# Kernel optimization log

Hardware: AMD Instinct MI355X
Metric: run time of the kernel (lower is better)

Reference implementation:

```python
import jax, jax.numpy as jnp
import numpy as np

EPS = 1e-6
ALPHA = 0.2  # LeakyReLU negative slope


def layer_norm(x, g, b):
    mu = jnp.mean(x, axis=-1, keepdims=True)
    var = jnp.mean(jnp.square(x - mu), axis=-1, keepdims=True)
    return (x - mu) * jax.lax.rsqrt(var + EPS) * g + b


def graph_attention(x, bias, W, a_src, a_dst):
    # x: [B,N,D], bias: [B,N,N], W: [D, H*Dh], a_src/a_dst: [H, Dh]
    B, N, D = x.shape
    H, Dh = a_src.shape
    h = jnp.einsum('bnd,dhk->bhnk', x, W.reshape(D, H, Dh))  # [B,H,N,Dh]
    s = jnp.einsum('bhnk,hk->bhn', h, a_src)                 # source term
    t = jnp.einsum('bhnk,hk->bhn', h, a_dst)                 # target term
    e = jax.nn.leaky_relu(s[:, :, :, None] + t[:, :, None, :], ALPHA)
    e = e + bias[:, None, :, :]                              # graph mask/bias
    attn = jax.nn.softmax(e, axis=-1)                        # [B,H,N,N]
    out = jnp.einsum('bhij,bhjk->bhik', attn, h)             # [B,H,N,Dh]
    return out.transpose(0, 2, 1, 3).reshape(B, N, H * Dh)


def setup_inputs() -> dict:
    key = jax.random.key(0)
    ks = jax.random.split(key, 8)
    B, N, D, H = 2, 2048, 512, 8
    Dh = D // H
    sc = 1.0 / np.sqrt(D)
    return {
        'x': jax.random.normal(ks[0], (B, N, D), jnp.float32),
        'bias': jax.random.normal(ks[1], (B, N, N), jnp.float32),
        'W1': jax.random.normal(ks[2], (D, D), jnp.float32) * sc,
        'a_src1': jax.random.normal(ks[3], (H, Dh), jnp.float32) * sc,
        'a_dst1': jax.random.normal(ks[4], (H, Dh), jnp.float32) * sc,
        'g1': jnp.ones((D,), jnp.float32),
        'b1': jnp.zeros((D,), jnp.float32),
        'W2': jax.random.normal(ks[5], (D, D), jnp.float32) * sc,
        'a_src2': jax.random.normal(ks[6], (1, D), jnp.float32) * sc,
        'a_dst2': jax.random.normal(ks[7], (1, D), jnp.float32) * sc,
        'g2': jnp.ones((D,), jnp.float32),
        'b2': jnp.zeros((D,), jnp.float32),
    }


def reference(x, bias, W1, a_src1, a_dst1, g1, b1, W2, a_src2, a_dst2, g2, b2):
    # dropout is identity in eval mode
    attn_in = layer_norm(x, g1, b1)
    attn = graph_attention(attn_in, bias, W1, a_src1, a_dst1) + x
    attn_in2 = layer_norm(attn, g2, b2)
    out = graph_attention(attn_in2, bias, W2, a_src2, a_dst2) + attn
    return out
```

## Files before the change

kernel.cpp:

```cpp
#include <hip/hip_runtime.h>
#include <math.h>

#define NB 2
#define NN 2048
#define DD 512
#define L2E 1.44269504088896340736f

typedef __attribute__((ext_vector_type(8))) short short8;
typedef __attribute__((ext_vector_type(4))) float f32x4;

__device__ __forceinline__ unsigned short f2bf(float x) {
  union { float f; unsigned u; } a;
  a.f = x;
  unsigned r = a.u + 0x7FFF + ((a.u >> 16) & 1);
  return (unsigned short)(r >> 16);
}
__device__ __forceinline__ float bf2f(unsigned short u) {
  union { unsigned u; float f; } a;
  a.u = ((unsigned)u) << 16;
  return a.f;
}
__device__ __forceinline__ unsigned cvtpk(float lo, float hi) {
  unsigned r;
  asm("v_cvt_pk_bf16_f32 %0, %1, %2" : "=v"(r) : "v"(lo), "v"(hi));
  return r;
}
__device__ __forceinline__ uint2 exp4pk(float e0, float e1, float e2, float e3) {
  float p0, p1, p2, p3;
  uint2 d;
  asm("v_exp_f32 %2, %6\n\t"
      "v_exp_f32 %3, %7\n\t"
      "v_exp_f32 %4, %8\n\t"
      "v_exp_f32 %5, %9\n\t"
      "v_cvt_pk_bf16_f32 %0, %2, %3\n\t"
      "v_cvt_pk_bf16_f32 %1, %4, %5"
      : "=&v"(d.x), "=&v"(d.y), "=&v"(p0), "=&v"(p1), "=&v"(p2), "=&v"(p3)
      : "v"(e0), "v"(e1), "v"(e2), "v"(e3));
  return d;
}

__device__ __forceinline__ float waveReduceSum(float v) {
#pragma unroll
  for (int o = 32; o; o >>= 1) v += __shfl_down(v, o, 64);
  return v;
}
__device__ __forceinline__ float blockReduceSum(float v, float* red4) {
  int tid = threadIdx.x;
  __syncthreads();
  v = waveReduceSum(v);
  if ((tid & 63) == 0) red4[tid >> 6] = v;
  __syncthreads();
  return red4[0] + red4[1] + red4[2] + red4[3];
}

__global__ __launch_bounds__(256) void prep_kernel(
    const float* __restrict__ W1, const float* __restrict__ W2,
    unsigned short* __restrict__ WT1, unsigned short* __restrict__ WT2,
    const float* __restrict__ as1, const float* __restrict__ ad1,
    float* __restrict__ vs1, float* __restrict__ vd1,
    const float* __restrict__ as2, const float* __restrict__ ad2,
    float* __restrict__ vs2, float* __restrict__ vd2) {
  __shared__ float tile[64][65];
  int bid = blockIdx.x;
  int t = threadIdx.x;
  if (bid < 128) {
    const float* W = (bid & 64) ? W2 : W1;
    unsigned short* WT = (bid & 64) ? WT2 : WT1;
    int r = bid & 63;
    int kt = (r >> 3) * 64, ct = (r & 7) * 64;
#pragma unroll
    for (int u = 0; u < 16; u++) {
      int lin = t + u * 256;
      int kl = lin >> 6, cl = lin & 63;
      tile[kl][cl] = W[(size_t)(kt + kl) * DD + ct + cl];
    }
    __syncthreads();
#pragma unroll
    for (int u = 0; u < 16; u++) {
      int lin = t + u * 256;
      int cl = lin >> 6, kl = lin & 63;
      WT[(size_t)(ct + cl) * DD + kt + kl] = f2bf(tile[kl][cl]);
    }
  } else {
    int idx = bid - 128;
    int slot = idx >> 3, dch = idx & 7;
    const float *W, *as, *ad;
    float *vs, *vd;
    int Dh, hoff;
    if (slot < 8) {
      W = W1; as = as1 + slot * 64; ad = ad1 + slot * 64;
      vs = vs1 + (size_t)slot * DD; vd = vd1 + (size_t)slot * DD;
      Dh = 64; hoff = slot * 64;
    } else {
      W = W2; as = as2; ad = ad2; vs = vs2; vd = vd2;
      Dh = 512; hoff = 0;
    }
    int dl = t >> 2, kq = t & 3;
    int d = dch * 64 + dl;
    int kn = Dh >> 2;
    const float* wr = W + (size_t)d * DD + hoff + kq * kn;
    const float* asp = as + kq * kn;
    const float* adp = ad + kq * kn;
    float s = 0.f, dd2 = 0.f;
    for (int k = 0; k < kn; k++) {
      float wv = wr[k];
      s += wv * asp[k];
      dd2 += wv * adp[k];
    }
    s += __shfl_xor(s, 1);
    s += __shfl_xor(s, 2);
    dd2 += __shfl_xor(dd2, 1);
    dd2 += __shfl_xor(dd2, 2);
    if (kq == 0) {
      vs[d] = s;
      vd[d] = dd2;
    }
  }
}

__global__ __launch_bounds__(256) void lnst_kernel(
    const float* __restrict__ x, const float* __restrict__ g,
    const float* __restrict__ bb, unsigned short* __restrict__ y,
    const float* __restrict__ vs, const float* __restrict__ vd,
    float* __restrict__ sOut, float* __restrict__ tOut, int HN) {
  __shared__ float red4[4];
  __shared__ float lnS[512];
  int row = blockIdx.x;
  int t = threadIdx.x;
  const float* xr = x + (size_t)row * DD;
  float2 v = *(const float2*)&xr[2 * t];
  float s = blockReduceSum(v.x + v.y, red4);
  float mu = s * (1.0f / 512.0f);
  float d0 = v.x - mu, d1 = v.y - mu;
  float ss = blockReduceSum(d0 * d0 + d1 * d1, red4);
  float rstd = rsqrtf(ss * (1.0f / 512.0f) + 1e-6f);
  float2 gg = *(const float2*)&g[2 * t];
  float2 bv = *(const float2*)&bb[2 * t];
  float n0 = d0 * rstd * gg.x + bv.x;
  float n1 = d1 * rstd * gg.y + bv.y;
  ushort2 o;
  o.x = f2bf(n0);
  o.y = f2bf(n1);
  *(ushort2*)&y[(size_t)row * DD + 2 * t] = o;
  lnS[2 * t] = n0;
  lnS[2 * t + 1] = n1;
  __syncthreads();
  int wv = t >> 6, l = t & 63;
  int b = row >> 11, n = row & (NN - 1);
  float4 x0 = *(const float4*)&lnS[l * 8];
  float4 x1 = *(const float4*)&lnS[l * 8 + 4];
  for (int h = wv; h < HN; h += 4) {
    const float* vsr = vs + (size_t)h * DD + l * 8;
    const float* vdr = vd + (size_t)h * DD + l * 8;
    float4 a0 = *(const float4*)vsr, a1 = *(const float4*)(vsr + 4);
    float4 c0 = *(const float4*)vdr, c1 = *(const float4*)(vdr + 4);
    float ps = x0.x * a0.x + x0.y * a0.y + x0.z * a0.z + x0.w * a0.w +
               x1.x * a1.x + x1.y * a1.y + x1.z * a1.z + x1.w * a1.w;
    float pd = x0.x * c0.x + x0.y * c0.y + x0.z * c0.z + x0.w * c0.w +
               x1.x * c1.x + x1.y * c1.y + x1.z * c1.z + x1.w * c1.w;
#pragma unroll
    for (int o2 = 32; o2; o2 >>= 1) {
      ps += __shfl_xor(ps, o2);
      pd += __shfl_xor(pd, o2);
    }
    if (l == 0) {
      sOut[((size_t)b * HN + h) * NN + n] = ps * L2E;
      tOut[((size_t)b * HN + h) * NN + n] = pd * L2E;
    }
  }
}

__global__ __launch_bounds__(256) void gemm_kernel(const unsigned short* __restrict__ A,
                                                   const unsigned short* __restrict__ BT,
                                                   unsigned short* __restrict__ hbT) {
  __shared__ float accL[4][16][65];
  int t = threadIdx.x, w = t >> 6, l = t & 63;
  int li = l & 15, lg = l >> 4;
  int R0 = blockIdx.x * 16;
  int c0 = blockIdx.y * 64;
  const unsigned short* ar = A + (size_t)(R0 + li) * DD + w * 128 + lg * 8;
  const unsigned short* br = BT + (size_t)(c0 + li) * DD + w * 128 + lg * 8;
  f32x4 acc[4] = {};
#pragma unroll
  for (int k0 = 0; k0 < 128; k0 += 32) {
    short8 af = *(const short8*)(ar + k0);
#pragma unroll
    for (int f = 0; f < 4; f++) {
      short8 bf = *(const short8*)(br + (size_t)f * 16 * DD + k0);
      acc[f] = __builtin_amdgcn_mfma_f32_16x16x32_bf16(af, bf, acc[f], 0, 0, 0);
    }
  }
#pragma unroll
  for (int f = 0; f < 4; f++)
#pragma unroll
    for (int r = 0; r < 4; r++) accL[w][lg * 4 + r][f * 16 + li] = acc[f][r];
  __syncthreads();
  int b = R0 >> 11, jT = (R0 & (NN - 1)) >> 4;
#pragma unroll
  for (int u = 0; u < 2; u++) {
    int idx = t + u * 256;
    int f = idx >> 7;
    int rem = idx & 127;
    int cl = rem >> 3, jlp = rem & 7;
    int cc = f * 16 + cl;
    float v0 = accL[0][2 * jlp][cc] + accL[1][2 * jlp][cc] + accL[2][2 * jlp][cc] +
               accL[3][2 * jlp][cc];
    float v1 = accL[0][2 * jlp + 1][cc] + accL[1][2 * jlp + 1][cc] +
               accL[2][2 * jlp + 1][cc] + accL[3][2 * jlp + 1][cc];
    size_t off = (((size_t)(b * (DD / 64) + blockIdx.y) * (NN / 16)) + jT) * 1024 +
                 f * 256 + cl * 16 + jlp * 2;
    *(unsigned*)(hbT + off) = cvtpk(v0, v1);
  }
}

__global__ __launch_bounds__(1024) void pvh_kernel(
    const unsigned short* __restrict__ hbT, const float* __restrict__ bias,
    const float* __restrict__ sArr, const float* __restrict__ tArr,
    const float* __restrict__ res, float* __restrict__ out) {
  __shared__ __align__(16) unsigned char smem[65536];
  unsigned short (*Pl)[2][1024] = (unsigned short (*)[2][1024])smem;
  int t = threadIdx.x, w = t >> 6, l = t & 63;
  int h = w & 7, jh = w >> 3;
  int li = l & 15, lg = l >> 4;
  int i0g = blockIdx.x * 16;
  int b = i0g >> 11, i0 = i0g & (NN - 1);
  size_t bhN = (size_t)(b * 8 + h) * NN;
  const float* trow = tArr + bhN;

  int rs = l >> 3, js = (l & 7) * 8, jc = l & 7;
  int wchunk = ((jc & 4) | ((jc & 3) ^ (rs & 3))) * 8;
  float sv[2];
  sv[0] = sArr[bhN + i0 + rs];
  sv[1] = sArr[bhN + i0 + 8 + rs];
  const float* bb0 = bias + ((size_t)b * NN + i0 + rs) * NN;
  const float* bb1 = bb0 + (size_t)8 * NN;

  const unsigned short* vbase =
      hbT + ((size_t)(b * 8 + h) * (NN / 16)) * 1024 + (lg >> 1) * 1024 + li * 16 +
      (lg & 1) * 8;
  int ra0 = li * 64 + (lg ^ (li & 3)) * 8;
  int ra1 = ra0 + 32;

  union { short8 v; unsigned short q[8]; } ones;
#pragma unroll
  for (int k = 0; k < 8; k++) ones.q[k] = 0x3F80;

  f32x4 acc[4] = {};
  f32x4 accS = {0.f, 0.f, 0.f, 0.f};

  auto loadTB = [&](int j, float4& t0, float4& t1, float4& b0a, float4& b0b,
                    float4& b1a, float4& b1b) {
    t0 = *(const float4*)&trow[j + js];
    t1 = *(const float4*)&trow[j + js + 4];
    b0a = *(const float4*)&bb0[j + js];
    b0b = *(const float4*)&bb0[j + js + 4];
    b1a = *(const float4*)&bb1[j + js];
    b1b = *(const float4*)&bb1[j + js + 4];
  };
  auto computeP = [&](const float4& t0, const float4& t1, const float4& b0a,
                      const float4& b0b, const float4& b1a, const float4& b1b, int pb) {
#pragma unroll
    for (int u = 0; u < 2; u++) {
      const float4& ba = u ? b1a : b0a;
      const float4& bc = u ? b1b : b0b;
      int row = u * 8 + rs;
      float e0 = sv[u] + t0.x, e1 = sv[u] + t0.y;
      float e2 = sv[u] + t0.z, e3 = sv[u] + t0.w;
      float e4 = sv[u] + t1.x, e5 = sv[u] + t1.y;
      float e6 = sv[u] + t1.z, e7 = sv[u] + t1.w;
      e0 = fmaf(ba.x, L2E, fmaxf(e0, 0.2f * e0));
      e1 = fmaf(ba.y, L2E, fmaxf(e1, 0.2f * e1));
      e2 = fmaf(ba.z, L2E, fmaxf(e2, 0.2f * e2));
      e3 = fmaf(ba.w, L2E, fmaxf(e3, 0.2f * e3));
      e4 = fmaf(bc.x, L2E, fmaxf(e4, 0.2f * e4));
      e5 = fmaf(bc.y, L2E, fmaxf(e5, 0.2f * e5));
      e6 = fmaf(bc.z, L2E, fmaxf(e6, 0.2f * e6));
      e7 = fmaf(bc.w, L2E, fmaxf(e7, 0.2f * e7));
      uint2 d0 = exp4pk(e0, e1, e2, e3);
      uint2 d1 = exp4pk(e4, e5, e6, e7);
      uint4 dd;
      dd.x = d0.x; dd.y = d0.y; dd.z = d1.x; dd.w = d1.y;
      *(uint4*)&Pl[w][pb][rs * 64 + u * 512 + wchunk] = dd;
    }
  };

  const int jbeg = jh * (NN / 2), jend = jbeg + NN / 2;
  float4 tA0, tA1, bA0, bA1, bA2, bA3;

  loadTB(jbeg, tA0, tA1, bA0, bA1, bA2, bA3);
  computeP(tA0, tA1, bA0, bA1, bA2, bA3, 0);
  loadTB(jbeg + 64, tA0, tA1, bA0, bA1, bA2, bA3);

  int buf = 0;
  for (int jt = jbeg; jt < jend; jt += 64) {
    const unsigned short* vp = vbase + (size_t)jt * 64;
    short8 v0 = *(const short8*)(vp + 0);
    short8 v1 = *(const short8*)(vp + 256);
    short8 v2 = *(const short8*)(vp + 512);
    short8 v3 = *(const short8*)(vp + 768);
    short8 v4 = *(const short8*)(vp + 2048);
    short8 v5 = *(const short8*)(vp + 2304);
    short8 v6 = *(const short8*)(vp + 2560);
    short8 v7 = *(const short8*)(vp + 2816);
    short8 a0 = *(const short8*)&Pl[w][buf][(li & 7) * 64 + (li >> 3) * 512 +
                                            ((lg ^ (li & 3)) * 8)];
    short8 a1 = *(const short8*)&Pl[w][buf][(li & 7) * 64 + (li >> 3) * 512 + 32 +
                                            ((lg ^ (li & 3)) * 8)];
    if (jt + 64 < jend) {
      float4 n0 = tA0, n1 = tA1, m0 = bA0, m1 = bA1, m2 = bA2, m3 = bA3;
      int jn = (jt + 128 < jend) ? (jt + 128) : jbeg;
      loadTB(jn, tA0, tA1, bA0, bA1, bA2, bA3);
      computeP(n0, n1, m0, m1, m2, m3, buf ^ 1);
    }
    __builtin_amdgcn_s_setprio(1);
    accS = __builtin_amdgcn_mfma_f32_16x16x32_bf16(a0, ones.v, accS, 0, 0, 0);
    acc[0] = __builtin_amdgcn_mfma_f32_16x16x32_bf16(a0, v0, acc[0], 0, 0, 0);
    acc[1] = __builtin_amdgcn_mfma_f32_16x16x32_bf16(a0, v1, acc[1], 0, 0, 0);
    acc[2] = __builtin_amdgcn_mfma_f32_16x16x32_bf16(a0, v2, acc[2], 0, 0, 0);
    acc[3] = __builtin_amdgcn_mfma_f32_16x16x32_bf16(a0, v3, acc[3], 0, 0, 0);
    accS = __builtin_amdgcn_mfma_f32_16x16x32_bf16(a1, ones.v, accS, 0, 0, 0);
    acc[0] = __builtin_amdgcn_mfma_f32_16x16x32_bf16(a1, v4, acc[0], 0, 0, 0);
    acc[1] = __builtin_amdgcn_mfma_f32_16x16x32_bf16(a1, v5, acc[1], 0, 0, 0);
    acc[2] = __builtin_amdgcn_mfma_f32_16x16x32_bf16(a1, v6, acc[2], 0, 0, 0);
    acc[3] = __builtin_amdgcn_mfma_f32_16x16x32_bf16(a1, v7, acc[3], 0, 0, 0);
    __builtin_amdgcn_s_setprio(0);
    buf ^= 1;
  }

  __syncthreads();
  float* mAcc = (float*)smem;
  float* mS = (float*)(smem + 8 * 16 * 68 * 4);
  if (jh == 1) {
#pragma unroll
    for (int f = 0; f < 4; f++)
#pragma unroll
      for (int r = 0; r < 4; r++)
        mAcc[((size_t)h * 16 + lg * 4 + r) * 68 + f * 16 + li] = acc[f][r];
    if (li == 0) {
#pragma unroll
      for (int r = 0; r < 4; r++) mS[h * 16 + lg * 4 + r] = accS[r];
    }
  }
  __syncthreads();
  if (jh == 0) {
#pragma unroll
    for (int r = 0; r < 4; r++) {
      float S = accS[r] + mS[h * 16 + lg * 4 + r];
      float inv = 1.0f / S;
      size_t ix = ((size_t)b * NN + i0 + lg * 4 + r) * DD + h * 64 + li;
#pragma unroll
      for (int f = 0; f < 4; f++) {
        float O = acc[f][r] + mAcc[((size_t)h * 16 + lg * 4 + r) * 68 + f * 16 + li];
        out[ix + f * 16] = O * inv + res[ix + f * 16];
      }
    }
  }
}

template <int HN, int CCH>
__global__ __launch_bounds__(256) void pv_kernel(
    const unsigned short* __restrict__ hbT, const float* __restrict__ bias,
    const float* __restrict__ sArr, const float* __restrict__ tArr,
    const float* __restrict__ res, float* __restrict__ out) {
  constexpr int DH = DD / HN;
  __shared__ unsigned short Pl[4][2][1024];
  __shared__ float accL[4][16][33];
  __shared__ float sLa[4][16];
  int t = threadIdx.x, w = t >> 6, l = t & 63;
  int li = l & 15, lg = l >> 4;
  int i0 = blockIdx.x * 16;
  int ck = blockIdx.y, bh = blockIdx.z;
  int h = bh % HN, b = bh / HN;
  int c0 = h * DH + ck * (CCH * 64);
  size_t bhN = (size_t)bh * NN;
  const float* trow = tArr + bhN;

  int rs = l >> 3, js = (l & 7) * 8, jc = l & 7;
  int wchunk = ((jc & 4) | ((jc & 3) ^ (rs & 3))) * 8;
  float sv[2];
  sv[0] = sArr[bhN + i0 + rs];
  sv[1] = sArr[bhN + i0 + 8 + rs];
  const float* bb0 = bias + ((size_t)b * NN + i0 + rs) * NN;
  const float* bb1 = bb0 + (size_t)8 * NN;

  const unsigned short* vbase =
      hbT + ((size_t)(b * (DD / 64) + (c0 >> 6)) * (NN / 16)) * 1024 +
      (lg >> 1) * 1024 + li * 16 + (lg & 1) * 8;
  int ra0 = li * 64 + (lg ^ (li & 3)) * 8;
  int ra1 = ra0 + 32;

  union { short8 v; unsigned short q[8]; } ones;
#pragma unroll
  for (int k = 0; k < 8; k++) ones.q[k] = 0x3F80;

  const int jbeg = w * (NN / 4), jend = jbeg + NN / 4;
  f32x4 acc[CCH][4] = {};
  f32x4 accS = {0.f, 0.f, 0.f, 0.f};

  auto loadTB = [&](int j, float4& t0, float4& t1, float4& b0a, float4& b0b,
                    float4& b1a, float4& b1b) {
    t0 = *(const float4*)&trow[j + js];
    t1 = *(const float4*)&trow[j + js + 4];
    b0a = *(const float4*)&bb0[j + js];
    b0b = *(const float4*)&bb0[j + js + 4];
    b1a = *(const float4*)&bb1[j + js];
    b1b = *(const float4*)&bb1[j + js + 4];
  };
  auto computeP = [&](const float4& t0, const float4& t1, const float4& b0a,
                      const float4& b0b, const float4& b1a, const float4& b1b, int pb) {
#pragma unroll
    for (int u = 0; u < 2; u++) {
      const float4& ba = u ? b1a : b0a;
      const float4& bc = u ? b1b : b0b;
      int row = u * 8 + rs;
      float e0 = sv[u] + t0.x, e1 = sv[u] + t0.y;
      float e2 = sv[u] + t0.z, e3 = sv[u] + t0.w;
      float e4 = sv[u] + t1.x, e5 = sv[u] + t1.y;
      float e6 = sv[u] + t1.z, e7 = sv[u] + t1.w;
      e0 = fmaf(ba.x, L2E, fmaxf(e0, 0.2f * e0));
      e1 = fmaf(ba.y, L2E, fmaxf(e1, 0.2f * e1));
      e2 = fmaf(ba.z, L2E, fmaxf(e2, 0.2f * e2));
      e3 = fmaf(ba.w, L2E, fmaxf(e3, 0.2f * e3));
      e4 = fmaf(bc.x, L2E, fmaxf(e4, 0.2f * e4));
      e5 = fmaf(bc.y, L2E, fmaxf(e5, 0.2f * e5));
      e6 = fmaf(bc.z, L2E, fmaxf(e6, 0.2f * e6));
      e7 = fmaf(bc.w, L2E, fmaxf(e7, 0.2f * e7));
      uint2 d0 = exp4pk(e0, e1, e2, e3);
      uint2 d1 = exp4pk(e4, e5, e6, e7);
      uint4 dd;
      dd.x = d0.x; dd.y = d0.y; dd.z = d1.x; dd.w = d1.y;
      *(uint4*)&Pl[w][pb][row * 64 + wchunk] = dd;
    }
  };

  float4 tA0, tA1, bA0, bA1, bA2, bA3;

  loadTB(jbeg, tA0, tA1, bA0, bA1, bA2, bA3);
  computeP(tA0, tA1, bA0, bA1, bA2, bA3, 0);
  loadTB(jbeg + 64, tA0, tA1, bA0, bA1, bA2, bA3);

  int buf = 0;
  for (int jt = jbeg; jt < jend; jt += 64) {
    short8 a0 = *(const short8*)&Pl[w][buf][ra0];
    short8 a1 = *(const short8*)&Pl[w][buf][ra1];
    if (jt + 64 < jend) {
      float4 n0 = tA0, n1 = tA1, m0 = bA0, m1 = bA1, m2 = bA2, m3 = bA3;
      int jn = (jt + 128 < jend) ? (jt + 128) : jbeg;
      loadTB(jn, tA0, tA1, bA0, bA1, bA2, bA3);
      computeP(n0, n1, m0, m1, m2, m3, buf ^ 1);
    }
    __builtin_amdgcn_s_setprio(1);
    accS = __builtin_amdgcn_mfma_f32_16x16x32_bf16(a0, ones.v, accS, 0, 0, 0);
    accS = __builtin_amdgcn_mfma_f32_16x16x32_bf16(a1, ones.v, accS, 0, 0, 0);
#pragma unroll
    for (int cc = 0; cc < CCH; cc++) {
      const unsigned short* vp =
          vbase + (size_t)cc * ((NN / 16) * 1024) + (size_t)jt * 64;
      short8 v0 = *(const short8*)(vp + 0);
      short8 v1 = *(const short8*)(vp + 256);
      short8 v2 = *(const short8*)(vp + 512);
      short8 v3 = *(const short8*)(vp + 768);
      acc[cc][0] = __builtin_amdgcn_mfma_f32_16x16x32_bf16(a0, v0, acc[cc][0], 0, 0, 0);
      acc[cc][1] = __builtin_amdgcn_mfma_f32_16x16x32_bf16(a0, v1, acc[cc][1], 0, 0, 0);
      acc[cc][2] = __builtin_amdgcn_mfma_f32_16x16x32_bf16(a0, v2, acc[cc][2], 0, 0, 0);
      acc[cc][3] = __builtin_amdgcn_mfma_f32_16x16x32_bf16(a0, v3, acc[cc][3], 0, 0, 0);
      short8 v4 = *(const short8*)(vp + 2048);
      short8 v5 = *(const short8*)(vp + 2304);
      short8 v6 = *(const short8*)(vp + 2560);
      short8 v7 = *(const short8*)(vp + 2816);
      acc[cc][0] = __builtin_amdgcn_mfma_f32_16x16x32_bf16(a1, v4, acc[cc][0], 0, 0, 0);
      acc[cc][1] = __builtin_amdgcn_mfma_f32_16x16x32_bf16(a1, v5, acc[cc][1], 0, 0, 0);
      acc[cc][2] = __builtin_amdgcn_mfma_f32_16x16x32_bf16(a1, v6, acc[cc][2], 0, 0, 0);
      acc[cc][3] = __builtin_amdgcn_mfma_f32_16x16x32_bf16(a1, v7, acc[cc][3], 0, 0, 0);
    }
    __builtin_amdgcn_s_setprio(0);
    buf ^= 1;
  }

  if (li == 0) {
#pragma unroll
    for (int r = 0; r < 4; r++) sLa[w][lg * 4 + r] = accS[r];
  }
#pragma unroll
  for (int g = 0; g < 2 * CCH; g++) {
    int cc = g >> 1, half = g & 1;
#pragma unroll
    for (int f = 0; f < 2; f++)
#pragma unroll
      for (int r = 0; r < 4; r++)
        accL[w][lg * 4 + r][f * 16 + li] = acc[cc][half * 2 + f][r];
    __syncthreads();
    {
      int rr = t >> 4, cp = (t & 15) * 2;
      float S = sLa[0][rr] + sLa[1][rr] + sLa[2][rr] + sLa[3][rr];
      float inv = 1.0f / S;
      float2 O = {0.f, 0.f};
#pragma unroll
      for (int w2 = 0; w2 < 4; w2++) {
        O.x += accL[w2][rr][cp];
        O.y += accL[w2][rr][cp + 1];
      }
      size_t ix = ((size_t)b * NN + i0 + rr) * DD + c0 + cc * 64 + half * 32 + cp;
      float2 rv = *(const float2*)&res[ix];
      float2 ov = {O.x * inv + rv.x, O.y * inv + rv.y};
      *(float2*)&out[ix] = ov;
    }
    __syncthreads();
  }
}

extern "C" void kernel_launch(void* const* d_in, const int* in_sizes, int n_in,
                              void* d_out, int out_size, void* d_ws, size_t ws_size,
                              hipStream_t stream) {
  const float* x = (const float*)d_in[0];
  const float* bias = (const float*)d_in[1];
  const float* W1 = (const float*)d_in[2];
  const float* asrc1 = (const float*)d_in[3];
  const float* adst1 = (const float*)d_in[4];
  const float* g1 = (const float*)d_in[5];
  const float* b1 = (const float*)d_in[6];
  const float* W2 = (const float*)d_in[7];
  const float* asrc2 = (const float*)d_in[8];
  const float* adst2 = (const float*)d_in[9];
  const float* g2 = (const float*)d_in[10];
  const float* b2 = (const float*)d_in[11];
  float* out = (float*)d_out;
  float* ws = (float*)d_ws;

  const size_t RC = (size_t)NB * NN * DD;
  float* attnBuf = ws;
  unsigned short* lnB = (unsigned short*)(ws + RC);
  unsigned short* hbT = (unsigned short*)(ws + RC + RC / 2);
  unsigned short* WT1 = (unsigned short*)(ws + 2 * RC);
  unsigned short* WT2 = WT1 + (size_t)DD * DD;
  float* vs1 = (float*)(WT2 + (size_t)DD * DD);
  float* vd1 = vs1 + 8 * DD;
  float* vs2 = vd1 + 8 * DD;
  float* vd2 = vs2 + DD;
  float* sBuf = vd2 + DD;
  float* tBuf = sBuf + 16 * NN;

  const int rows = NB * NN;

  hipLaunchKernelGGL(prep_kernel, dim3(128 + 72), dim3(256), 0, stream, W1, W2, WT1, WT2,
                     asrc1, adst1, vs1, vd1, asrc2, adst2, vs2, vd2);

  hipLaunchKernelGGL(lnst_kernel, dim3(rows), dim3(256), 0, stream, x, g1, b1, lnB, vs1, vd1,
                     sBuf, tBuf, 8);
  hipLaunchKernelGGL(gemm_kernel, dim3(256, 8), dim3(256), 0, stream, lnB, WT1, hbT);
  hipLaunchKernelGGL(pvh_kernel, dim3(256), dim3(1024), 0, stream, hbT, bias, sBuf, tBuf, x,
                     attnBuf);

  hipLaunchKernelGGL(lnst_kernel, dim3(rows), dim3(256), 0, stream, attnBuf, g2, b2, lnB, vs2,
                     vd2, sBuf, tBuf, 1);
  hipLaunchKernelGGL(gemm_kernel, dim3(256, 8), dim3(256), 0, stream, lnB, WT2, hbT);
  hipLaunchKernelGGL((pv_kernel<1, 4>), dim3(128, 2, 2), dim3(256), 0, stream, hbT, bias,
                     sBuf, tBuf, attnBuf, out);
}
```

Measured before the change: 174.0 us.

## Split attention kernels into smaller 256-thread blocks across heads and channel chunks

The first-layer attention kernel goes from 1024-thread blocks covering all 8 heads to 256-thread blocks covering 2 heads each, on a 3D grid with less shared memory. The second-layer kernel halves the channel chunk per block (CCH 4 to 2) and doubles the grid. It also prefetches all V fragments before the MFMAs and reuses the P buffer space for the reduction. This is meant to raise occupancy and block count so the SMs fill better and memory latency is hidden. The cost is recomputing the softmax weights (bias reads and exps) across more blocks, which means more bias traffic.

Result: faster. 152.2 us, median of 3 (-12.6%).

```diff
diff --git a/kernel.cpp b/kernel.cpp
--- a/kernel.cpp
+++ b/kernel.cpp
@@ -213,18 +213,21 @@
   }
 }
 
-__global__ __launch_bounds__(1024) void pvh_kernel(
+__global__ __launch_bounds__(256) void pvg_kernel(
     const unsigned short* __restrict__ hbT, const float* __restrict__ bias,
     const float* __restrict__ sArr, const float* __restrict__ tArr,
     const float* __restrict__ res, float* __restrict__ out) {
-  __shared__ __align__(16) unsigned char smem[65536];
+  __shared__ __align__(16) unsigned char smem[16896];
   unsigned short (*Pl)[2][1024] = (unsigned short (*)[2][1024])smem;
+  float (*accL2)[16][65] = (float (*)[16][65])smem;
+  float (*sLa)[16] = (float (*)[16])(smem + 8320);
   int t = threadIdx.x, w = t >> 6, l = t & 63;
-  int h = w & 7, jh = w >> 3;
+  int jh = w & 1, hp = w >> 1;
   int li = l & 15, lg = l >> 4;
-  int i0g = blockIdx.x * 16;
-  int b = i0g >> 11, i0 = i0g & (NN - 1);
-  size_t bhN = (size_t)(b * 8 + h) * NN;
+  int i0 = blockIdx.x * 16;
+  int h0 = blockIdx.y * 2, b = blockIdx.z;
+  int head = h0 + hp;
+  size_t bhN = (size_t)(b * 8 + head) * NN;
   const float* trow = tArr + bhN;
 
   int rs = l >> 3, js = (l & 7) * 8, jc = l & 7;
@@ -236,7 +239,7 @@
   const float* bb1 = bb0 + (size_t)8 * NN;
 
   const unsigned short* vbase =
-      hbT + ((size_t)(b * 8 + h) * (NN / 16)) * 1024 + (lg >> 1) * 1024 + li * 16 +
+      hbT + ((size_t)(b * 8 + head) * (NN / 16)) * 1024 + (lg >> 1) * 1024 + li * 16 +
       (lg & 1) * 8;
   int ra0 = li * 64 + (lg ^ (li & 3)) * 8;
   int ra1 = ra0 + 32;
@@ -245,156 +248,8 @@
 #pragma unroll
   for (int k = 0; k < 8; k++) ones.q[k] = 0x3F80;
 
+  const int jbeg = jh * (NN / 2), jend = jbeg + NN / 2;
   f32x4 acc[4] = {};
-  f32x4 accS = {0.f, 0.f, 0.f, 0.f};
-
-  auto loadTB = [&](int j, float4& t0, float4& t1, float4& b0a, float4& b0b,
-                    float4& b1a, float4& b1b) {
-    t0 = *(const float4*)&trow[j + js];
-    t1 = *(const float4*)&trow[j + js + 4];
-    b0a = *(const float4*)&bb0[j + js];
-    b0b = *(const float4*)&bb0[j + js + 4];
-    b1a = *(const float4*)&bb1[j + js];
-    b1b = *(const float4*)&bb1[j + js + 4];
-  };
-  auto computeP = [&](const float4& t0, const float4& t1, const float4& b0a,
-                      const float4& b0b, const float4& b1a, const float4& b1b, int pb) {
-#pragma unroll
-    for (int u = 0; u < 2; u++) {
-      const float4& ba = u ? b1a : b0a;
-      const float4& bc = u ? b1b : b0b;
-      int row = u * 8 + rs;
-      float e0 = sv[u] + t0.x, e1 = sv[u] + t0.y;
-      float e2 = sv[u] + t0.z, e3 = sv[u] + t0.w;
-      float e4 = sv[u] + t1.x, e5 = sv[u] + t1.y;
-      float e6 = sv[u] + t1.z, e7 = sv[u] + t1.w;
-      e0 = fmaf(ba.x, L2E, fmaxf(e0, 0.2f * e0));
-      e1 = fmaf(ba.y, L2E, fmaxf(e1, 0.2f * e1));
-      e2 = fmaf(ba.z, L2E, fmaxf(e2, 0.2f * e2));
-      e3 = fmaf(ba.w, L2E, fmaxf(e3, 0.2f * e3));
-      e4 = fmaf(bc.x, L2E, fmaxf(e4, 0.2f * e4));
-      e5 = fmaf(bc.y, L2E, fmaxf(e5, 0.2f * e5));
-      e6 = fmaf(bc.z, L2E, fmaxf(e6, 0.2f * e6));
-      e7 = fmaf(bc.w, L2E, fmaxf(e7, 0.2f * e7));
-      uint2 d0 = exp4pk(e0, e1, e2, e3);
-      uint2 d1 = exp4pk(e4, e5, e6, e7);
-      uint4 dd;
-      dd.x = d0.x; dd.y = d0.y; dd.z = d1.x; dd.w = d1.y;
-      *(uint4*)&Pl[w][pb][rs * 64 + u * 512 + wchunk] = dd;
-    }
-  };
-
-  const int jbeg = jh * (NN / 2), jend = jbeg + NN / 2;
-  float4 tA0, tA1, bA0, bA1, bA2, bA3;
-
-  loadTB(jbeg, tA0, tA1, bA0, bA1, bA2, bA3);
-  computeP(tA0, tA1, bA0, bA1, bA2, bA3, 0);
-  loadTB(jbeg + 64, tA0, tA1, bA0, bA1, bA2, bA3);
-
-  int buf = 0;
-  for (int jt = jbeg; jt < jend; jt += 64) {
-    const unsigned short* vp = vbase + (size_t)jt * 64;
-    short8 v0 = *(const short8*)(vp + 0);
-    short8 v1 = *(const short8*)(vp + 256);
-    short8 v2 = *(const short8*)(vp + 512);
-    short8 v3 = *(const short8*)(vp + 768);
-    short8 v4 = *(const short8*)(vp + 2048);
-    short8 v5 = *(const short8*)(vp + 2304);
-    short8 v6 = *(const short8*)(vp + 2560);
-    short8 v7 = *(const short8*)(vp + 2816);
-    short8 a0 = *(const short8*)&Pl[w][buf][(li & 7) * 64 + (li >> 3) * 512 +
-                                            ((lg ^ (li & 3)) * 8)];
-    short8 a1 = *(const short8*)&Pl[w][buf][(li & 7) * 64 + (li >> 3) * 512 + 32 +
-                                            ((lg ^ (li & 3)) * 8)];
-    if (jt + 64 < jend) {
-      float4 n0 = tA0, n1 = tA1, m0 = bA0, m1 = bA1, m2 = bA2, m3 = bA3;
-      int jn = (jt + 128 < jend) ? (jt + 128) : jbeg;
-      loadTB(jn, tA0, tA1, bA0, bA1, bA2, bA3);
-      computeP(n0, n1, m0, m1, m2, m3, buf ^ 1);
-    }
-    __builtin_amdgcn_s_setprio(1);
-    accS = __builtin_amdgcn_mfma_f32_16x16x32_bf16(a0, ones.v, accS, 0, 0, 0);
-    acc[0] = __builtin_amdgcn_mfma_f32_16x16x32_bf16(a0, v0, acc[0], 0, 0, 0);
-    acc[1] = __builtin_amdgcn_mfma_f32_16x16x32_bf16(a0, v1, acc[1], 0, 0, 0);
-    acc[2] = __builtin_amdgcn_mfma_f32_16x16x32_bf16(a0, v2, acc[2], 0, 0, 0);
-    acc[3] = __builtin_amdgcn_mfma_f32_16x16x32_bf16(a0, v3, acc[3], 0, 0, 0);
-    accS = __builtin_amdgcn_mfma_f32_16x16x32_bf16(a1, ones.v, accS, 0, 0, 0);
-    acc[0] = __builtin_amdgcn_mfma_f32_16x16x32_bf16(a1, v4, acc[0], 0, 0, 0);
-    acc[1] = __builtin_amdgcn_mfma_f32_16x16x32_bf16(a1, v5, acc[1], 0, 0, 0);
-    acc[2] = __builtin_amdgcn_mfma_f32_16x16x32_bf16(a1, v6, acc[2], 0, 0, 0);
-    acc[3] = __builtin_amdgcn_mfma_f32_16x16x32_bf16(a1, v7, acc[3], 0, 0, 0);
-    __builtin_amdgcn_s_setprio(0);
-    buf ^= 1;
-  }
-
-  __syncthreads();
-  float* mAcc = (float*)smem;
-  float* mS = (float*)(smem + 8 * 16 * 68 * 4);
-  if (jh == 1) {
-#pragma unroll
-    for (int f = 0; f < 4; f++)
-#pragma unroll
-      for (int r = 0; r < 4; r++)
-        mAcc[((size_t)h * 16 + lg * 4 + r) * 68 + f * 16 + li] = acc[f][r];
-    if (li == 0) {
-#pragma unroll
-      for (int r = 0; r < 4; r++) mS[h * 16 + lg * 4 + r] = accS[r];
-    }
-  }
-  __syncthreads();
-  if (jh == 0) {
-#pragma unroll
-    for (int r = 0; r < 4; r++) {
-      float S = accS[r] + mS[h * 16 + lg * 4 + r];
-      float inv = 1.0f / S;
-      size_t ix = ((size_t)b * NN + i0 + lg * 4 + r) * DD + h * 64 + li;
-#pragma unroll
-      for (int f = 0; f < 4; f++) {
-        float O = acc[f][r] + mAcc[((size_t)h * 16 + lg * 4 + r) * 68 + f * 16 + li];
-        out[ix + f * 16] = O * inv + res[ix + f * 16];
-      }
-    }
-  }
-}
-
-template <int HN, int CCH>
-__global__ __launch_bounds__(256) void pv_kernel(
-    const unsigned short* __restrict__ hbT, const float* __restrict__ bias,
-    const float* __restrict__ sArr, const float* __restrict__ tArr,
-    const float* __restrict__ res, float* __restrict__ out) {
-  constexpr int DH = DD / HN;
-  __shared__ unsigned short Pl[4][2][1024];
-  __shared__ float accL[4][16][33];
-  __shared__ float sLa[4][16];
-  int t = threadIdx.x, w = t >> 6, l = t & 63;
-  int li = l & 15, lg = l >> 4;
-  int i0 = blockIdx.x * 16;
-  int ck = blockIdx.y, bh = blockIdx.z;
-  int h = bh % HN, b = bh / HN;
-  int c0 = h * DH + ck * (CCH * 64);
-  size_t bhN = (size_t)bh * NN;
-  const float* trow = tArr + bhN;
-
-  int rs = l >> 3, js = (l & 7) * 8, jc = l & 7;
-  int wchunk = ((jc & 4) | ((jc & 3) ^ (rs & 3))) * 8;
-  float sv[2];
-  sv[0] = sArr[bhN + i0 + rs];
-  sv[1] = sArr[bhN + i0 + 8 + rs];
-  const float* bb0 = bias + ((size_t)b * NN + i0 + rs) * NN;
-  const float* bb1 = bb0 + (size_t)8 * NN;
-
-  const unsigned short* vbase =
-      hbT + ((size_t)(b * (DD / 64) + (c0 >> 6)) * (NN / 16)) * 1024 +
-      (lg >> 1) * 1024 + li * 16 + (lg & 1) * 8;
-  int ra0 = li * 64 + (lg ^ (li & 3)) * 8;
-  int ra1 = ra0 + 32;
-
-  union { short8 v; unsigned short q[8]; } ones;
-#pragma unroll
-  for (int k = 0; k < 8; k++) ones.q[k] = 0x3F80;
-
-  const int jbeg = w * (NN / 4), jend = jbeg + NN / 4;
-  f32x4 acc[CCH][4] = {};
   f32x4 accS = {0.f, 0.f, 0.f, 0.f};
 
   auto loadTB = [&](int j, float4& t0, float4& t1, float4& b0a, float4& b0b,
@@ -441,6 +296,15 @@
 
   int buf = 0;
   for (int jt = jbeg; jt < jend; jt += 64) {
+    const unsigned short* vp = vbase + (size_t)jt * 64;
+    short8 v0 = *(const short8*)(vp + 0);
+    short8 v1 = *(const short8*)(vp + 256);
+    short8 v2 = *(const short8*)(vp + 512);
+    short8 v3 = *(const short8*)(vp + 768);
+    short8 v4 = *(const short8*)(vp + 2048);
+    short8 v5 = *(const short8*)(vp + 2304);
+    short8 v6 = *(const short8*)(vp + 2560);
+    short8 v7 = *(const short8*)(vp + 2816);
     short8 a0 = *(const short8*)&Pl[w][buf][ra0];
     short8 a1 = *(const short8*)&Pl[w][buf][ra1];
     if (jt + 64 < jend) {
@@ -451,32 +315,179 @@
     }
     __builtin_amdgcn_s_setprio(1);
     accS = __builtin_amdgcn_mfma_f32_16x16x32_bf16(a0, ones.v, accS, 0, 0, 0);
+    acc[0] = __builtin_amdgcn_mfma_f32_16x16x32_bf16(a0, v0, acc[0], 0, 0, 0);
+    acc[1] = __builtin_amdgcn_mfma_f32_16x16x32_bf16(a0, v1, acc[1], 0, 0, 0);
+    acc[2] = __builtin_amdgcn_mfma_f32_16x16x32_bf16(a0, v2, acc[2], 0, 0, 0);
+    acc[3] = __builtin_amdgcn_mfma_f32_16x16x32_bf16(a0, v3, acc[3], 0, 0, 0);
     accS = __builtin_amdgcn_mfma_f32_16x16x32_bf16(a1, ones.v, accS, 0, 0, 0);
+    acc[0] = __builtin_amdgcn_mfma_f32_16x16x32_bf16(a1, v4, acc[0], 0, 0, 0);
+    acc[1] = __builtin_amdgcn_mfma_f32_16x16x32_bf16(a1, v5, acc[1], 0, 0, 0);
+    acc[2] = __builtin_amdgcn_mfma_f32_16x16x32_bf16(a1, v6, acc[2], 0, 0, 0);
+    acc[3] = __builtin_amdgcn_mfma_f32_16x16x32_bf16(a1, v7, acc[3], 0, 0, 0);
+    __builtin_amdgcn_s_setprio(0);
+    buf ^= 1;
+  }
+
+  __syncthreads();
+  if (li == 0) {
+#pragma unroll
+    for (int r = 0; r < 4; r++) sLa[w][lg * 4 + r] = accS[r];
+  }
+#pragma unroll
+  for (int hp2 = 0; hp2 < 2; hp2++) {
+    if (hp == hp2) {
+#pragma unroll
+      for (int f = 0; f < 4; f++)
+#pragma unroll
+        for (int r = 0; r < 4; r++) accL2[jh][lg * 4 + r][f * 16 + li] = acc[f][r];
+    }
+    __syncthreads();
+    {
+      int rr = t >> 4, cq = t & 15;
+      float S = sLa[2 * hp2][rr] + sLa[2 * hp2 + 1][rr];
+      float inv = 1.0f / S;
+      size_t ixb = ((size_t)b * NN + i0 + rr) * DD + (h0 + hp2) * 64 + cq;
+#pragma unroll
+      for (int f = 0; f < 4; f++) {
+        int col = f * 16 + cq;
+        float O = accL2[0][rr][col] + accL2[1][rr][col];
+        out[ixb + f * 16] = O * inv + res[ixb + f * 16];
+      }
+    }
+    __syncthreads();
+  }
+}
+
+template <int HN, int CCH>
+__global__ __launch_bounds__(256) void pv_kernel(
+    const unsigned short* __restrict__ hbT, const float* __restrict__ bias,
+    const float* __restrict__ sArr, const float* __restrict__ tArr,
+    const float* __restrict__ res, float* __restrict__ out) {
+  constexpr int DH = DD / HN;
+  __shared__ __align__(16) unsigned char smem[16640];
+  unsigned short (*Pl)[2][1024] = (unsigned short (*)[2][1024])smem;
+  float (*accL)[16][33] = (float (*)[16][33])smem;
+  float (*sLa)[16] = (float (*)[16])(smem + 8448);
+  int t = threadIdx.x, w = t >> 6, l = t & 63;
+  int li = l & 15, lg = l >> 4;
+  int i0 = blockIdx.x * 16;
+  int ck = blockIdx.y, bh = blockIdx.z;
+  int h = bh % HN, b = bh / HN;
+  int c0 = h * DH + ck * (CCH * 64);
+  size_t bhN = (size_t)bh * NN;
+  const float* trow = tArr + bhN;
+
+  int rs = l >> 3, js = (l & 7) * 8, jc = l & 7;
+  int wchunk = ((jc & 4) | ((jc & 3) ^ (rs & 3))) * 8;
+  float sv[2];
+  sv[0] = sArr[bhN + i0 + rs];
+  sv[1] = sArr[bhN + i0 + 8 + rs];
+  const float* bb0 = bias + ((size_t)b * NN + i0 + rs) * NN;
+  const float* bb1 = bb0 + (size_t)8 * NN;
+
+  const unsigned short* vbase =
+      hbT + ((size_t)(b * (DD / 64) + (c0 >> 6)) * (NN / 16)) * 1024 +
+      (lg >> 1) * 1024 + li * 16 + (lg & 1) * 8;
+  int ra0 = li * 64 + (lg ^ (li & 3)) * 8;
+  int ra1 = ra0 + 32;
+
+  union { short8 v; unsigned short q[8]; } ones;
+#pragma unroll
+  for (int k = 0; k < 8; k++) ones.q[k] = 0x3F80;
+
+  const int jbeg = w * (NN / 4), jend = jbeg + NN / 4;
+  f32x4 acc[CCH][4] = {};
+  f32x4 accS = {0.f, 0.f, 0.f, 0.f};
+
+  auto loadTB = [&](int j, float4& t0, float4& t1, float4& b0a, float4& b0b,
+                    float4& b1a, float4& b1b) {
+    t0 = *(const float4*)&trow[j + js];
+    t1 = *(const float4*)&trow[j + js + 4];
+    b0a = *(const float4*)&bb0[j + js];
+    b0b = *(const float4*)&bb0[j + js + 4];
+    b1a = *(const float4*)&bb1[j + js];
+    b1b = *(const float4*)&bb1[j + js + 4];
+  };
+  auto computeP = [&](const float4& t0, const float4& t1, const float4& b0a,
+                      const float4& b0b, const float4& b1a, const float4& b1b, int pb) {
+#pragma unroll
+    for (int u = 0; u < 2; u++) {
+      const float4& ba = u ? b1a : b0a;
+      const float4& bc = u ? b1b : b0b;
+      int row = u * 8 + rs;
+      float e0 = sv[u] + t0.x, e1 = sv[u] + t0.y;
+      float e2 = sv[u] + t0.z, e3 = sv[u] + t0.w;
+      float e4 = sv[u] + t1.x, e5 = sv[u] + t1.y;
+      float e6 = sv[u] + t1.z, e7 = sv[u] + t1.w;
+      e0 = fmaf(ba.x, L2E, fmaxf(e0, 0.2f * e0));
+      e1 = fmaf(ba.y, L2E, fmaxf(e1, 0.2f * e1));
+      e2 = fmaf(ba.z, L2E, fmaxf(e2, 0.2f * e2));
+      e3 = fmaf(ba.w, L2E, fmaxf(e3, 0.2f * e3));
+      e4 = fmaf(bc.x, L2E, fmaxf(e4, 0.2f * e4));
+      e5 = fmaf(bc.y, L2E, fmaxf(e5, 0.2f * e5));
+      e6 = fmaf(bc.z, L2E, fmaxf(e6, 0.2f * e6));
+      e7 = fmaf(bc.w, L2E, fmaxf(e7, 0.2f * e7));
+      uint2 d0 = exp4pk(e0, e1, e2, e3);
+      uint2 d1 = exp4pk(e4, e5, e6, e7);
+      uint4 dd;
+      dd.x = d0.x; dd.y = d0.y; dd.z = d1.x; dd.w = d1.y;
+      *(uint4*)&Pl[w][pb][row * 64 + wchunk] = dd;
+    }
+  };
+  auto loadV = [&](int jt, short8 (&vv)[CCH][8]) {
 #pragma unroll
     for (int cc = 0; cc < CCH; cc++) {
       const unsigned short* vp =
           vbase + (size_t)cc * ((NN / 16) * 1024) + (size_t)jt * 64;
-      short8 v0 = *(const short8*)(vp + 0);
-      short8 v1 = *(const short8*)(vp + 256);
-      short8 v2 = *(const short8*)(vp + 512);
-      short8 v3 = *(const short8*)(vp + 768);
-      acc[cc][0] = __builtin_amdgcn_mfma_f32_16x16x32_bf16(a0, v0, acc[cc][0], 0, 0, 0);
-      acc[cc][1] = __builtin_amdgcn_mfma_f32_16x16x32_bf16(a0, v1, acc[cc][1], 0, 0, 0);
-      acc[cc][2] = __builtin_amdgcn_mfma_f32_16x16x32_bf16(a0, v2, acc[cc][2], 0, 0, 0);
-      acc[cc][3] = __builtin_amdgcn_mfma_f32_16x16x32_bf16(a0, v3, acc[cc][3], 0, 0, 0);
-      short8 v4 = *(const short8*)(vp + 2048);
-      short8 v5 = *(const short8*)(vp + 2304);
-      short8 v6 = *(const short8*)(vp + 2560);
-      short8 v7 = *(const short8*)(vp + 2816);
-      acc[cc][0] = __builtin_amdgcn_mfma_f32_16x16x32_bf16(a1, v4, acc[cc][0], 0, 0, 0);
-      acc[cc][1] = __builtin_amdgcn_mfma_f32_16x16x32_bf16(a1, v5, acc[cc][1], 0, 0, 0);
-      acc[cc][2] = __builtin_amdgcn_mfma_f32_16x16x32_bf16(a1, v6, acc[cc][2], 0, 0, 0);
-      acc[cc][3] = __builtin_amdgcn_mfma_f32_16x16x32_bf16(a1, v7, acc[cc][3], 0, 0, 0);
-    }
+#pragma unroll
+      for (int f = 0; f < 4; f++) {
+        vv[cc][f] = *(const short8*)(vp + f * 256);
+        vv[cc][4 + f] = *(const short8*)(vp + 2048 + f * 256);
+      }
+    }
+  };
+  auto domfma = [&](short8 a0, short8 a1, const short8 (&vv)[CCH][8]) {
+    __builtin_amdgcn_s_setprio(1);
+    accS = __builtin_amdgcn_mfma_f32_16x16x32_bf16(a0, ones.v, accS, 0, 0, 0);
+#pragma unroll
+    for (int cc = 0; cc < CCH; cc++)
+#pragma unroll
+      for (int f = 0; f < 4; f++)
+        acc[cc][f] =
+            __builtin_amdgcn_mfma_f32_16x16x32_bf16(a0, vv[cc][f], acc[cc][f], 0, 0, 0);
+    accS = __builtin_amdgcn_mfma_f32_16x16x32_bf16(a1, ones.v, accS, 0, 0, 0);
+#pragma unroll
+    for (int cc = 0; cc < CCH; cc++)
+#pragma unroll
+      for (int f = 0; f < 4; f++)
+        acc[cc][f] =
+            __builtin_amdgcn_mfma_f32_16x16x32_bf16(a1, vv[cc][4 + f], acc[cc][f], 0, 0, 0);
     __builtin_amdgcn_s_setprio(0);
+  };
+
+  float4 tA0, tA1, bA0, bA1, bA2, bA3;
+  short8 vv[CCH][8];
+
+  loadTB(jbeg, tA0, tA1, bA0, bA1, bA2, bA3);
+  computeP(tA0, tA1, bA0, bA1, bA2, bA3, 0);
+  loadTB(jbeg + 64, tA0, tA1, bA0, bA1, bA2, bA3);
+
+  int buf = 0;
+  for (int jt = jbeg; jt < jend; jt += 64) {
+    loadV(jt, vv);
+    short8 a0 = *(const short8*)&Pl[w][buf][ra0];
+    short8 a1 = *(const short8*)&Pl[w][buf][ra1];
+    if (jt + 64 < jend) {
+      float4 n0 = tA0, n1 = tA1, m0 = bA0, m1 = bA1, m2 = bA2, m3 = bA3;
+      int jn = (jt + 128 < jend) ? (jt + 128) : jbeg;
+      loadTB(jn, tA0, tA1, bA0, bA1, bA2, bA3);
+      computeP(n0, n1, m0, m1, m2, m3, buf ^ 1);
+    }
+    domfma(a0, a1, vv);
     buf ^= 1;
   }
 
+  __syncthreads();
   if (li == 0) {
 #pragma unroll
     for (int r = 0; r < 4; r++) sLa[w][lg * 4 + r] = accS[r];
@@ -548,12 +559,12 @@
   hipLaunchKernelGGL(lnst_kernel, dim3(rows), dim3(256), 0, stream, x, g1, b1, lnB, vs1, vd1,
                      sBuf, tBuf, 8);
   hipLaunchKernelGGL(gemm_kernel, dim3(256, 8), dim3(256), 0, stream, lnB, WT1, hbT);
-  hipLaunchKernelGGL(pvh_kernel, dim3(256), dim3(1024), 0, stream, hbT, bias, sBuf, tBuf, x,
-                     attnBuf);
+  hipLaunchKernelGGL(pvg_kernel, dim3(128, 4, 2), dim3(256), 0, stream, hbT, bias, sBuf,
+                     tBuf, x, attnBuf);
 
   hipLaunchKernelGGL(lnst_kernel, dim3(rows), dim3(256), 0, stream, attnBuf, g2, b2, lnB, vs2,
                      vd2, sBuf, tBuf, 1);
   hipLaunchKernelGGL(gemm_kernel, dim3(256, 8), dim3(256), 0, stream, lnB, WT2, hbT);
-  hipLaunchKernelGGL((pv_kernel<1, 4>), dim3(128, 2, 2), dim3(256), 0, stream, hbT, bias,
+  hipLaunchKernelGGL((pv_kernel<1, 2>), dim3(128, 4, 2), dim3(256), 0, stream, hbT, bias,
                      sBuf, tBuf, attnBuf, out);
 }
```
